# Performance work log

Measured on AMD Instinct MI355X. Metric: run time of the kernel, lower is better.

Reference implementation:

```python
import jax, jax.numpy as jnp
import numpy as np
from jax import lax

SCALE = 1.0 / np.sqrt(1500.0)  # self.dim = sqrt(1500)


def conv1d(x, w, b, stride, padding):
    # x: [B, Cin, L], w: [Cout, Cin, K] (torch layout)
    y = lax.conv_general_dilated(x, w, (stride,), padding,
                                 dimension_numbers=('NCH', 'OIH', 'NCH'))
    return y + b[None, :, None]


def setup_inputs() -> dict:
    key = jax.random.key(0)
    ks = jax.random.split(key, 16)
    B, L, F = 32, 1500, 8  # feature_len = 8, seq len pinned by sqrt(1500) and logit=Linear(176,3)

    def n(k, shape, s=0.1):
        return jax.random.normal(k, shape, jnp.float32) * s

    return {
        'signal': jax.random.normal(ks[0], (B, 1, L), jnp.float32),
        # first (and only executed) head: kernel_size = 3, padding 'same'
        'wq': n(ks[1], (F, 1, 3)), 'bq': n(ks[2], (F,)),
        'wk': n(ks[3], (F, 1, 3)), 'bk': n(ks[4], (F,)),
        'wv': n(ks[5], (F, 1, 3)), 'bv': n(ks[6], (F,)),
        # final conv stack (finetune path): 1500 -> 374 -> 92 -> 22
        'w1': n(ks[7], (32, F, 8)),  'b1': n(ks[8], (32,)),
        'w2': n(ks[9], (64, 32, 8)), 'b2': n(ks[10], (64,)),
        'w3': n(ks[11], (F, 64, 8)), 'b3': n(ks[12], (F,)),
        # logit: Linear(176, 3); 176 = 8 * 22
        'wl': n(ks[13], (3, 176)), 'bl': n(ks[14], (3,)),
    }


def reference(signal, wq, bq, wk, bk, wv, bv, w1, b1, w2, b2, w3, b3, wl, bl):
    # conv QKV projections (kernel 3, 'same' padding), each [B, 8, L]
    Q = conv1d(signal, wq, bq, 1, 'SAME')
    K = conv1d(signal, wk, bk, 1, 'SAME')
    V = conv1d(signal, wv, bv, 1, 'SAME')
    # score = bmm(Q^T, K) / sqrt(1500)  -> [B, L, L]
    score = jnp.einsum('bcl,bcm->blm', Q, K) * SCALE
    attn = jax.nn.softmax(score, axis=-1)
    # context = bmm(attn, V^T)^T -> [B, 8, L]
    context = jnp.einsum('blm,bcm->bcl', attn, V)
    # finetune head: three strided convs (no activations in the original)
    h = conv1d(context, w1, b1, 4, 'VALID')  # [B, 32, 374]
    h = conv1d(h, w2, b2, 4, 'VALID')        # [B, 64, 92]
    h = conv1d(h, w3, b3, 4, 'VALID')        # [B, 8, 22]
    flat = h.reshape(h.shape[0], -1)          # [B, 176]
    return flat @ wl.T + bl                   # [B, 3]
```

## Files before the change

kernel.cpp:

```cpp
#include <hip/hip_runtime.h>

#define F_SCALE 0.02581988897471611f
#define F_LOG2E 1.4426950408889634f

constexpr int B_ = 32;
constexpr int L_ = 1500;

#define ACC4(A, s, e) \
    A.x = fmaf(s, e.x, A.x); A.y = fmaf(s, e.y, A.y); \
    A.z = fmaf(s, e.z, A.z); A.w = fmaf(s, e.w, A.w)

__global__ __launch_bounds__(512) void fused_all(
    const float* __restrict__ signal,
    const float* __restrict__ wq, const float* __restrict__ bq,
    const float* __restrict__ wk,
    const float* __restrict__ wv, const float* __restrict__ bv,
    const float* __restrict__ w1, const float* __restrict__ b1,
    const float* __restrict__ w2, const float* __restrict__ b2,
    const float* __restrict__ w3, const float* __restrict__ b3,
    const float* __restrict__ wl, const float* __restrict__ bl,
    float* __restrict__ out)
{
    __shared__ float  sw[1504];
    __shared__ float4 umq[3500];
    __shared__ float4 Gacc4[20];
    __shared__ float4 h1q[32*94];
    __shared__ float  flat[176];

    float4* const h2q = umq;
    float*  const red = (float*)h1q;

    const int tid = threadIdx.x;
    const int b   = blockIdx.x;
    const int wid = tid >> 6;
    const int ln  = tid & 63;
    const float* sgb = signal + (size_t)b * L_;

    for (int i = tid; i < 1504; i += 512) {
        const int gi = i - 1;
        sw[i] = (gi >= 0 && gi < L_) ? sgb[gi] : 0.0f;
    }
    float Mm[9], uu[3];
    #pragma unroll
    for (int a = 0; a < 3; a++) {
        #pragma unroll
        for (int d = 0; d < 3; d++) {
            float acc = 0.0f;
            #pragma unroll
            for (int c = 0; c < 8; c++) acc += wq[c*3+a] * wk[c*3+d];
            Mm[a*3+d] = acc * F_SCALE;
        }
    }
    #pragma unroll
    for (int d = 0; d < 3; d++) {
        float acc = 0.0f;
        #pragma unroll
        for (int c = 0; c < 8; c++) acc += bq[c] * wk[c*3+d];
        uu[d] = acc * (F_SCALE * F_LOG2E);
    }
    __syncthreads();

    float4 aq0 = make_float4(0,0,0,0), aq1 = aq0, aq2 = aq0, aq3 = aq0;

    for (int chk = 0; chk < 3; ++chk) {
        const int m0 = chk * 500;
        if (tid < 500) {
            const int j = tid;
            const float x0 = sw[m0+j], x1 = sw[m0+j+1], x2 = sw[m0+j+2];
            const float h0  = Mm[0]*x0 + Mm[1]*x1 + Mm[2]*x2;
            const float h1v = Mm[3]*x0 + Mm[4]*x1 + Mm[5]*x2;
            const float h2v = Mm[6]*x0 + Mm[7]*x1 + Mm[8]*x2;
            const float E   = __builtin_amdgcn_exp2f(uu[0]*x0 + uu[1]*x1 + uu[2]*x2);
            const float p00=h0*h0, p01=h0*h1v, p02=h0*h2v;
            const float p11=h1v*h1v, p12=h1v*h2v, p22=h2v*h2v;
            float4* row = &umq[j*7];
            row[0] = make_float4(E*x0, E*x1, E*x2, E);
            row[1] = make_float4(h0, h1v, h2v, p00);
            row[2] = make_float4(p01, p02, p11, p12);
            row[3] = make_float4(p22, h0*p00, h1v*p00, h2v*p00);
            row[4] = make_float4(h0*p11, h0*p12, h0*p22, h1v*p11);
            row[5] = make_float4(h2v*p11, h1v*p22, h2v*p22, 1.0f);
        }
        __syncthreads();
        if (wid < 5) {
            #pragma unroll
            for (int ii = 0; ii < 8; ++ii) {
                const int j = ln + 64*ii;
                if (j < 500) {
                    const float4 ex = umq[j*7];
                    const float4 mq = umq[j*7 + 1 + wid];
                    ACC4(aq0, mq.x, ex); ACC4(aq1, mq.y, ex);
                    ACC4(aq2, mq.z, ex); ACC4(aq3, mq.w, ex);
                }
            }
        }
        __syncthreads();
    }

    if (wid < 5) {
        float4* rp = (float4*)&red[(wid*64 + ln)*20];
        rp[0] = aq0; rp[1] = aq1; rp[2] = aq2; rp[3] = aq3;
    }
    __syncthreads();
    if (tid < 80) {
        const int jm = tid >> 2, cc = tid & 3;
        int grp, qq;
        if (jm == 0)      { grp = 4; qq = 3; }
        else if (jm < 17) { grp = (jm-1) >> 2; qq = (jm-1) & 3; }
        else              { grp = 4; qq = jm - 17; }
        const float* rb = red + (size_t)grp*64*20 + qq*4 + cc;
        float val = 0.0f;
        #pragma unroll 8
        for (int l = 0; l < 64; ++l) val += rb[l*20];
        ((float*)Gacc4)[tid] = val;
    }
    __syncthreads();

    for (int l = tid; l < 1500; l += 512) {
        const float y0 = sw[l], y1 = sw[l+1], y2 = sw[l+2];
        const float t00=y0*y0, t01=y0*y1, t02=y0*y2, t11=y1*y1, t12=y1*y2, t22=y2*y2;
        const float c6 = 1.0f/6.0f;
        float ym[20];
        ym[0]=1.0f; ym[1]=y0; ym[2]=y1; ym[3]=y2;
        ym[4]=0.5f*t00; ym[5]=t01; ym[6]=t02; ym[7]=0.5f*t11; ym[8]=t12; ym[9]=0.5f*t22;
        ym[10]=c6*(y0*t00);  ym[11]=0.5f*(y1*t00); ym[12]=0.5f*(y2*t00);
        ym[13]=0.5f*(y0*t11); ym[14]=y0*t12;       ym[15]=0.5f*(y0*t22);
        ym[16]=c6*(y1*t11);  ym[17]=0.5f*(y2*t11); ym[18]=0.5f*(y1*t22);
        ym[19]=c6*(y2*t22);
        float4 S = make_float4(0,0,0,0);
        #pragma unroll
        for (int jj = 0; jj < 20; ++jj) {
            const float4 G = Gacc4[jj];
            ACC4(S, ym[jj], G);
        }
        const float rd = 1.0f / S.w;
        umq[l] = make_float4(S.x*rd, S.y*rd, S.z*rd, 0.0f);
    }

    {
        const int o = tid & 31, g = tid >> 5;
        float A[8][3];
        float b1p = b1[o];
        #pragma unroll
        for (int k = 0; k < 8; ++k) { A[k][0]=0.f; A[k][1]=0.f; A[k][2]=0.f; }
        #pragma unroll
        for (int i = 0; i < 8; ++i) {
            const float v0 = wv[i*3+0], v1 = wv[i*3+1], v2 = wv[i*3+2];
            const float bvi = bv[i];
            #pragma unroll
            for (int k = 0; k < 8; ++k) {
                const float w = w1[o*64 + i*8 + k];
                A[k][0] = fmaf(w, v0, A[k][0]);
                A[k][1] = fmaf(w, v1, A[k][1]);
                A[k][2] = fmaf(w, v2, A[k][2]);
                b1p     = fmaf(w, bvi, b1p);
            }
        }
        __syncthreads();
        const float4* TD = umq;
        float* h1f = (float*)h1q;
        for (int t = g; t < 374; t += 16) {
            float acc = b1p;
            const int li = 4*t;
            #pragma unroll
            for (int k = 0; k < 8; ++k) {
                const float4 T = TD[li + k];
                acc += A[k][0]*T.x + A[k][1]*T.y + A[k][2]*T.z;
            }
            h1f[o*376 + t] = acc;
        }
    }
    __syncthreads();

    {
        const int og = tid >> 5;
        const int ts = tid & 31;
        const int ob = 4*og;
        float acc2[3][4];
        #pragma unroll
        for (int j = 0; j < 3; ++j) {
            #pragma unroll
            for (int q = 0; q < 4; ++q) acc2[j][q] = b2[ob+q];
        }
        const float4* w2q4 = (const float4*)w2;
        #pragma unroll 2
        for (int i = 0; i < 32; ++i) {
            float4 wA[4], wB[4];
            #pragma unroll
            for (int q = 0; q < 4; ++q) {
                wA[q] = w2q4[(ob+q)*64 + 2*i];
                wB[q] = w2q4[(ob+q)*64 + 2*i + 1];
            }
            #pragma unroll
            for (int j = 0; j < 3; ++j) {
                const int t = ts + 32*j;
                if (t < 92) {
                    const float4 a0 = h1q[i*94 + t];
                    const float4 a1 = h1q[i*94 + t + 1];
                    #pragma unroll
                    for (int q = 0; q < 4; ++q) {
                        acc2[j][q] += a0.x*wA[q].x + a0.y*wA[q].y + a0.z*wA[q].z + a0.w*wA[q].w
                                    + a1.x*wB[q].x + a1.y*wB[q].y + a1.z*wB[q].z + a1.w*wB[q].w;
                    }
                }
            }
        }
        float* h2f = (float*)h2q;
        #pragma unroll
        for (int j = 0; j < 3; ++j) {
            const int t = ts + 32*j;
            if (t < 92) {
                #pragma unroll
                for (int q = 0; q < 4; ++q) h2f[(ob+q)*96 + t] = acc2[j][q];
            }
        }
    }
    __syncthreads();

    if (tid < 176) {
        const int c3 = tid / 22, t = tid - c3*22;
        float acc = b3[c3];
        #pragma unroll 8
        for (int i = 0; i < 64; ++i) {
            const float4 a0 = h2q[i*24 + t];
            const float4 a1 = h2q[i*24 + t + 1];
            const float* w = w3 + (c3*64 + i)*8;
            acc += a0.x*w[0] + a0.y*w[1] + a0.z*w[2] + a0.w*w[3]
                 + a1.x*w[4] + a1.y*w[5] + a1.z*w[6] + a1.w*w[7];
        }
        flat[tid] = acc;
    }
    __syncthreads();
    if (tid < 192) {
        float acc = 0.0f;
        for (int n = ln; n < 176; n += 64) acc += flat[n] * wl[wid*176 + n];
        #pragma unroll
        for (int off = 32; off; off >>= 1) acc += __shfl_xor(acc, off, 64);
        if (ln == 0) out[b*3 + wid] = acc + bl[wid];
    }
}

extern "C" void kernel_launch(void* const* d_in, const int* in_sizes, int n_in,
                              void* d_out, int out_size, void* d_ws, size_t ws_size,
                              hipStream_t stream) {
    const float* signal = (const float*)d_in[0];
    const float* wq = (const float*)d_in[1];  const float* bq = (const float*)d_in[2];
    const float* wk = (const float*)d_in[3];
    const float* wvp = (const float*)d_in[5]; const float* bv = (const float*)d_in[6];
    const float* w1 = (const float*)d_in[7];  const float* b1 = (const float*)d_in[8];
    const float* w2 = (const float*)d_in[9];  const float* b2 = (const float*)d_in[10];
    const float* w3 = (const float*)d_in[11]; const float* b3 = (const float*)d_in[12];
    const float* wl = (const float*)d_in[13]; const float* bl = (const float*)d_in[14];
    float* out = (float*)d_out;
    (void)d_ws; (void)ws_size;

    hipLaunchKernelGGL(fused_all, dim3(B_), dim3(512), 0, stream,
                       signal, wq, bq, wk, wvp, bv, w1, b1, w2, b2, w3, b3, wl, bl, out);
}
```

Before: 121.1 us.

## Split each batch across four blocks and move conv3/logit to second kernel

```diff
diff --git a/kernel.cpp b/kernel.cpp
--- a/kernel.cpp
+++ b/kernel.cpp
@@ -10,28 +10,25 @@
     A.x = fmaf(s, e.x, A.x); A.y = fmaf(s, e.y, A.y); \
     A.z = fmaf(s, e.z, A.z); A.w = fmaf(s, e.w, A.w)
 
-__global__ __launch_bounds__(512) void fused_all(
+__global__ __launch_bounds__(512) void main_k(
     const float* __restrict__ signal,
     const float* __restrict__ wq, const float* __restrict__ bq,
     const float* __restrict__ wk,
     const float* __restrict__ wv, const float* __restrict__ bv,
     const float* __restrict__ w1, const float* __restrict__ b1,
     const float* __restrict__ w2, const float* __restrict__ b2,
-    const float* __restrict__ w3, const float* __restrict__ b3,
-    const float* __restrict__ wl, const float* __restrict__ bl,
-    float* __restrict__ out)
+    float* __restrict__ h2)
 {
     __shared__ float  sw[1504];
     __shared__ float4 umq[3500];
-    __shared__ float4 Gacc4[20];
-    __shared__ float4 h1q[32*94];
-    __shared__ float  flat[176];
-
-    float4* const h2q = umq;
-    float*  const red = (float*)h1q;
+    __shared__ float  red[6400];
+    __shared__ float4 Gs4[20];
+    __shared__ float4 TDs[392];
+    __shared__ float  h1s[32 * 100];
 
     const int tid = threadIdx.x;
-    const int b   = blockIdx.x;
+    const int xs  = blockIdx.x;
+    const int b   = blockIdx.y;
     const int wid = tid >> 6;
     const int ln  = tid & 63;
     const float* sgb = signal + (size_t)b * L_;
@@ -40,6 +37,7 @@
         const int gi = i - 1;
         sw[i] = (gi >= 0 && gi < L_) ? sgb[gi] : 0.0f;
     }
+
     float Mm[9], uu[3];
     #pragma unroll
     for (int a = 0; a < 3; a++) {
@@ -58,10 +56,27 @@
         for (int c = 0; c < 8; c++) acc += bq[c] * wk[c*3+d];
         uu[d] = acc * (F_SCALE * F_LOG2E);
     }
+    const int o31 = tid & 31;
+    float A[8][3];
+    float b1p = b1[o31];
+    #pragma unroll
+    for (int k = 0; k < 8; ++k) { A[k][0]=0.f; A[k][1]=0.f; A[k][2]=0.f; }
+    #pragma unroll
+    for (int i = 0; i < 8; ++i) {
+        const float v0 = wv[i*3+0], v1 = wv[i*3+1], v2 = wv[i*3+2];
+        const float bvi = bv[i];
+        #pragma unroll
+        for (int k = 0; k < 8; ++k) {
+            const float w = w1[o31*64 + i*8 + k];
+            A[k][0] = fmaf(w, v0, A[k][0]);
+            A[k][1] = fmaf(w, v1, A[k][1]);
+            A[k][2] = fmaf(w, v2, A[k][2]);
+            b1p     = fmaf(w, bvi, b1p);
+        }
+    }
     __syncthreads();
 
     float4 aq0 = make_float4(0,0,0,0), aq1 = aq0, aq2 = aq0, aq3 = aq0;
-
     for (int chk = 0; chk < 3; ++chk) {
         const int m0 = chk * 500;
         if (tid < 500) {
@@ -96,7 +111,6 @@
         }
         __syncthreads();
     }
-
     if (wid < 5) {
         float4* rp = (float4*)&red[(wid*64 + ln)*20];
         rp[0] = aq0; rp[1] = aq1; rp[2] = aq2; rp[3] = aq3;
@@ -112,11 +126,12 @@
         float val = 0.0f;
         #pragma unroll 8
         for (int l = 0; l < 64; ++l) val += rb[l*20];
-        ((float*)Gacc4)[tid] = val;
-    }
-    __syncthreads();
-
-    for (int l = tid; l < 1500; l += 512) {
+        ((float*)Gs4)[tid] = val;
+    }
+    __syncthreads();
+
+    if (tid < 388) {
+        const int l = 368*xs + tid;
         const float y0 = sw[l], y1 = sw[l+1], y2 = sw[l+2];
         const float t00=y0*y0, t01=y0*y1, t02=y0*y2, t11=y1*y1, t12=y1*y2, t22=y2*y2;
         const float c6 = 1.0f/6.0f;
@@ -130,113 +145,82 @@
         float4 S = make_float4(0,0,0,0);
         #pragma unroll
         for (int jj = 0; jj < 20; ++jj) {
-            const float4 G = Gacc4[jj];
+            const float4 G = Gs4[jj];
             ACC4(S, ym[jj], G);
         }
         const float rd = 1.0f / S.w;
-        umq[l] = make_float4(S.x*rd, S.y*rd, S.z*rd, 0.0f);
-    }
+        TDs[tid] = make_float4(S.x*rd, S.y*rd, S.z*rd, 0.0f);
+    }
+    __syncthreads();
 
     {
-        const int o = tid & 31, g = tid >> 5;
-        float A[8][3];
-        float b1p = b1[o];
-        #pragma unroll
-        for (int k = 0; k < 8; ++k) { A[k][0]=0.f; A[k][1]=0.f; A[k][2]=0.f; }
-        #pragma unroll
-        for (int i = 0; i < 8; ++i) {
-            const float v0 = wv[i*3+0], v1 = wv[i*3+1], v2 = wv[i*3+2];
-            const float bvi = bv[i];
+        const int cg = tid >> 5;
+        for (int c = cg; c < 96; c += 16) {
+            float acc = b1p;
             #pragma unroll
             for (int k = 0; k < 8; ++k) {
-                const float w = w1[o*64 + i*8 + k];
-                A[k][0] = fmaf(w, v0, A[k][0]);
-                A[k][1] = fmaf(w, v1, A[k][1]);
-                A[k][2] = fmaf(w, v2, A[k][2]);
-                b1p     = fmaf(w, bvi, b1p);
-            }
-        }
-        __syncthreads();
-        const float4* TD = umq;
-        float* h1f = (float*)h1q;
-        for (int t = g; t < 374; t += 16) {
-            float acc = b1p;
-            const int li = 4*t;
-            #pragma unroll
-            for (int k = 0; k < 8; ++k) {
-                const float4 T = TD[li + k];
+                const float4 T = TDs[4*c + k];
                 acc += A[k][0]*T.x + A[k][1]*T.y + A[k][2]*T.z;
             }
-            h1f[o*376 + t] = acc;
+            h1s[o31*100 + c] = acc;
         }
     }
     __syncthreads();
 
     {
-        const int og = tid >> 5;
+        const int op = tid >> 5;
         const int ts = tid & 31;
-        const int ob = 4*og;
-        float acc2[3][4];
-        #pragma unroll
-        for (int j = 0; j < 3; ++j) {
-            #pragma unroll
-            for (int q = 0; q < 4; ++q) acc2[j][q] = b2[ob+q];
-        }
-        const float4* w2q4 = (const float4*)w2;
-        #pragma unroll 2
-        for (int i = 0; i < 32; ++i) {
-            float4 wA[4], wB[4];
-            #pragma unroll
-            for (int q = 0; q < 4; ++q) {
-                wA[q] = w2q4[(ob+q)*64 + 2*i];
-                wB[q] = w2q4[(ob+q)*64 + 2*i + 1];
-            }
-            #pragma unroll
-            for (int j = 0; j < 3; ++j) {
-                const int t = ts + 32*j;
-                if (t < 92) {
-                    const float4 a0 = h1q[i*94 + t];
-                    const float4 a1 = h1q[i*94 + t + 1];
-                    #pragma unroll
-                    for (int q = 0; q < 4; ++q) {
-                        acc2[j][q] += a0.x*wA[q].x + a0.y*wA[q].y + a0.z*wA[q].z + a0.w*wA[q].w
-                                    + a1.x*wB[q].x + a1.y*wB[q].y + a1.z*wB[q].z + a1.w*wB[q].w;
-                    }
+        if (ts < 23) {
+            float acc[4];
+            #pragma unroll
+            for (int q = 0; q < 4; ++q) acc[q] = b2[op + 16*q];
+            const float4* w2q4 = (const float4*)w2;
+            const float4* h1s4 = (const float4*)h1s;
+            #pragma unroll 4
+            for (int i = 0; i < 32; ++i) {
+                const float4 a0 = h1s4[i*25 + ts];
+                const float4 a1 = h1s4[i*25 + ts + 1];
+                #pragma unroll
+                for (int q = 0; q < 4; ++q) {
+                    const float4 wA = w2q4[(op+16*q)*64 + 2*i];
+                    const float4 wB = w2q4[(op+16*q)*64 + 2*i + 1];
+                    acc[q] += a0.x*wA.x + a0.y*wA.y + a0.z*wA.z + a0.w*wA.w
+                            + a1.x*wB.x + a1.y*wB.y + a1.z*wB.z + a1.w*wB.w;
                 }
             }
-        }
-        float* h2f = (float*)h2q;
-        #pragma unroll
-        for (int j = 0; j < 3; ++j) {
-            const int t = ts + 32*j;
-            if (t < 92) {
-                #pragma unroll
-                for (int q = 0; q < 4; ++q) h2f[(ob+q)*96 + t] = acc2[j][q];
-            }
-        }
-    }
-    __syncthreads();
-
+            #pragma unroll
+            for (int q = 0; q < 4; ++q)
+                h2[((size_t)b*64 + op + 16*q)*96 + 23*xs + ts] = acc[q];
+        }
+    }
+}
+
+__global__ __launch_bounds__(192) void conv3_logit(
+    const float* __restrict__ h2, const float* __restrict__ w3,
+    const float* __restrict__ b3, const float* __restrict__ wl,
+    const float* __restrict__ bl, float* __restrict__ out)
+{
+    __shared__ float flat[176];
+    const int tid = threadIdx.x, b = blockIdx.x;
     if (tid < 176) {
-        const int c3 = tid / 22, t = tid - c3*22;
-        float acc = b3[c3];
+        const int c = tid / 22, t = tid % 22;
+        float acc = b3[c];
+        const float4* hb = reinterpret_cast<const float4*>(h2 + (size_t)b * 64 * 96);
         #pragma unroll 8
-        for (int i = 0; i < 64; ++i) {
-            const float4 a0 = h2q[i*24 + t];
-            const float4 a1 = h2q[i*24 + t + 1];
-            const float* w = w3 + (c3*64 + i)*8;
+        for (int i = 0; i < 64; i++) {
+            const float4 a0 = hb[i * 24 + t];
+            const float4 a1 = hb[i * 24 + t + 1];
+            const float* w = w3 + (c * 64 + i) * 8;
             acc += a0.x*w[0] + a0.y*w[1] + a0.z*w[2] + a0.w*w[3]
                  + a1.x*w[4] + a1.y*w[5] + a1.z*w[6] + a1.w*w[7];
         }
         flat[tid] = acc;
     }
     __syncthreads();
-    if (tid < 192) {
-        float acc = 0.0f;
-        for (int n = ln; n < 176; n += 64) acc += flat[n] * wl[wid*176 + n];
-        #pragma unroll
-        for (int off = 32; off; off >>= 1) acc += __shfl_xor(acc, off, 64);
-        if (ln == 0) out[b*3 + wid] = acc + bl[wid];
+    if (tid < 3) {
+        float acc = bl[tid];
+        for (int n = 0; n < 176; n++) acc += flat[n] * wl[tid * 176 + n];
+        out[b * 3 + tid] = acc;
     }
 }
 
@@ -246,14 +230,17 @@
     const float* signal = (const float*)d_in[0];
     const float* wq = (const float*)d_in[1];  const float* bq = (const float*)d_in[2];
     const float* wk = (const float*)d_in[3];
-    const float* wvp = (const float*)d_in[5]; const float* bv = (const float*)d_in[6];
+    const float* wv = (const float*)d_in[5];  const float* bv = (const float*)d_in[6];
     const float* w1 = (const float*)d_in[7];  const float* b1 = (const float*)d_in[8];
     const float* w2 = (const float*)d_in[9];  const float* b2 = (const float*)d_in[10];
     const float* w3 = (const float*)d_in[11]; const float* b3 = (const float*)d_in[12];
     const float* wl = (const float*)d_in[13]; const float* bl = (const float*)d_in[14];
     float* out = (float*)d_out;
-    (void)d_ws; (void)ws_size;
-
-    hipLaunchKernelGGL(fused_all, dim3(B_), dim3(512), 0, stream,
-                       signal, wq, bq, wk, wvp, bv, w1, b1, w2, b2, w3, b3, wl, bl, out);
+
+    float* h2 = (float*)d_ws;
+
+    hipLaunchKernelGGL(main_k, dim3(4, 32), dim3(512), 0, stream,
+                       signal, wq, bq, wk, wv, bv, w1, b1, w2, b2, h2);
+    hipLaunchKernelGGL(conv3_logit, dim3(32), dim3(192), 0, stream,
+                       h2, w3, b3, wl, bl, out);
 }
```

Measured after the change: 126.0 us. +4.1%, slower.
